# Kernel optimization log

Hardware: AMD Instinct MI355X
Metric: run time of the kernel (lower is better)

## Reference

```python
import jax, jax.numpy as jnp
import numpy as np
from jax.ops import segment_sum

N = 100000   # nodes
E = 1600000  # edges
F = 128      # node feature dim
H = 128      # hidden dim
FE = 16      # edge feature dim
G = 256      # num graphs
EPS = 1e-5   # batch-norm eps


def setup_inputs() -> dict:
    key = jax.random.key(0)
    ks = jax.random.split(key, 16)
    s = 0.05
    return {
        "x": jax.random.normal(ks[0], (N, F), jnp.float32),
        "edge_index": jax.random.randint(ks[1], (2, E), 0, N, dtype=jnp.int32),
        "edge_attr": jax.random.normal(ks[2], (E, FE), jnp.float32),
        "batch_idx": jnp.sort(jax.random.randint(ks[3], (N,), 0, G, dtype=jnp.int32)),
        # GCN layer 1
        "W_g1": jax.random.normal(ks[4], (F, H), jnp.float32) * s,
        "b_g1": jnp.zeros((H,), jnp.float32),
        "gamma1": jnp.ones((H,), jnp.float32),
        "beta1": jnp.zeros((H,), jnp.float32),
        # GCN layer 2
        "W_g2": jax.random.normal(ks[5], (H, H), jnp.float32) * s,
        "b_g2": jnp.zeros((H,), jnp.float32),
        "gamma2": jnp.ones((H,), jnp.float32),
        "beta2": jnp.zeros((H,), jnp.float32),
        # edge encoder MLP
        "W_e1": jax.random.normal(ks[6], (FE, H), jnp.float32) * s,
        "b_e1": jnp.zeros((H,), jnp.float32),
        "W_e2": jax.random.normal(ks[7], (H, H), jnp.float32) * s,
        "b_e2": jnp.zeros((H,), jnp.float32),
    }


def _gcn_bn_relu(x, src, dst, W, b, gamma, beta):
    """GCNConv (sym-normalized, self-loops) + BatchNorm1d (batch stats) + ReLU."""
    h = x @ W                                             # [N, H]
    ones = jnp.ones((E,), h.dtype)
    deg = segment_sum(ones, dst, num_segments=N) + 1.0    # self-loop degree
    dinv = jax.lax.rsqrt(deg)                             # [N]
    norm = dinv[src] * dinv[dst]                          # [E]
    agg = segment_sum(h[src] * norm[:, None], dst, num_segments=N)
    out = agg + h * (dinv * dinv)[:, None] + b            # self-loop + bias
    mu = out.mean(axis=0)
    var = out.var(axis=0)
    out = (out - mu) * jax.lax.rsqrt(var + EPS) * gamma + beta
    return jax.nn.relu(out)


def reference(x, edge_index, edge_attr, batch_idx, W_g1, b_g1, gamma1, beta1,
              W_g2, b_g2, gamma2, beta2, W_e1, b_e1, W_e2, b_e2):
    src, dst = edge_index[0], edge_index[1]
    h = _gcn_bn_relu(x, src, dst, W_g1, b_g1, gamma1, beta1)
    h = _gcn_bn_relu(h, src, dst, W_g2, b_g2, gamma2, beta2)

    # global mean pool over nodes per graph
    node_cnt = segment_sum(jnp.ones((N,), h.dtype), batch_idx, num_segments=G)
    graph_repr = segment_sum(h, batch_idx, num_segments=G) / jnp.maximum(node_cnt, 1.0)[:, None]

    # edge encoder MLP + per-graph edge mean (vectorized version of the loop)
    e = jax.nn.relu(edge_attr @ W_e1 + b_e1) @ W_e2 + b_e2   # [E, H]
    edge_batch = batch_idx[src]                              # [E]
    edge_cnt = segment_sum(jnp.ones((E,), e.dtype), edge_batch, num_segments=G)
    edge_sum = segment_sum(e, edge_batch, num_segments=G)
    edge_repr = jnp.where(edge_cnt[:, None] > 0, edge_sum / jnp.maximum(edge_cnt, 1.0)[:, None], 0.0)

    return graph_repr + edge_repr  # [G, H]
```

## Files before the change

kernel.cpp:

```cpp
#include <hip/hip_runtime.h>
#include <cstdint>

__device__ inline unsigned int bfpack2(float a, float b) {
  unsigned int ua = __float_as_uint(a), ub = __float_as_uint(b);
  ua += 0x7FFFu + ((ua >> 16) & 1u);
  ub += 0x7FFFu + ((ub >> 16) & 1u);
  return (ua >> 16) | (ub & 0xFFFF0000u);
}
__device__ inline float bflo(unsigned int u) { return __uint_as_float(u << 16); }
__device__ inline float bfhi(unsigned int u) { return __uint_as_float(u & 0xFFFF0000u); }

__global__ __launch_bounds__(256) void pre_kernel(const int* __restrict__ src,
                                                  const int* __restrict__ dst,
                                                  int* __restrict__ deg,
                                                  int* __restrict__ deg2, int nE) {
  int e = blockIdx.x * 256 + threadIdx.x;
  if (e < nE) {
    atomicAdd(&deg[dst[e]], 1);
    atomicAdd(&deg2[src[e]], 1);
  }
}

__global__ __launch_bounds__(256) void scanA_kernel(const int* __restrict__ deg,
                                                    const int* __restrict__ deg2,
                                                    int* __restrict__ rp,
                                                    int* __restrict__ rp2,
                                                    int* __restrict__ part,
                                                    int* __restrict__ part2,
                                                    int n, int nb) {
  __shared__ int sh[256];
  int b = blockIdx.x, t = threadIdx.x;
  const int* d = (b < nb) ? deg : deg2;
  int* r = (b < nb) ? rp : rp2;
  int* p = (b < nb) ? part : part2;
  int pad = (b < nb) ? 1 : 0;
  int bb = (b < nb) ? b : b - nb;
  int base = bb * 1024 + t * 4;
  int v0 = (base + 0 < n) ? d[base + 0] : 0;
  int v1 = (base + 1 < n) ? d[base + 1] : 0;
  int v2 = (base + 2 < n) ? d[base + 2] : 0;
  int v3 = (base + 3 < n) ? d[base + 3] : 0;
  if (pad) {
    v0 = (v0 + 7) & ~7; v1 = (v1 + 7) & ~7;
    v2 = (v2 + 7) & ~7; v3 = (v3 + 7) & ~7;
  }
  int ts = v0 + v1 + v2 + v3;
  sh[t] = ts;
  __syncthreads();
  for (int off = 1; off < 256; off <<= 1) {
    int x = (t >= off) ? sh[t - off] : 0;
    __syncthreads();
    sh[t] += x;
    __syncthreads();
  }
  int excl = sh[t] - ts;
  if (t == 255) p[bb] = sh[255];
  if (base + 0 < n) r[base + 0] = excl;
  if (base + 1 < n) r[base + 1] = excl + v0;
  if (base + 2 < n) r[base + 2] = excl + v0 + v1;
  if (base + 3 < n) r[base + 3] = excl + v0 + v1 + v2;
}

__global__ void scanB_kernel(int* part, int* part2, int* rp, int* rp2, int nb, int n) {
  if (threadIdx.x == 0) {
    int* p = (blockIdx.x == 0) ? part : part2;
    int* r = (blockIdx.x == 0) ? rp : rp2;
    int run = 0;
    for (int i = 0; i < nb; ++i) { int v = p[i]; p[i] = run; run += v; }
    r[n] = run;
  }
}

__global__ __launch_bounds__(256) void scanC_kernel(int* __restrict__ rp,
                                                    int* __restrict__ rp2,
                                                    const int* __restrict__ part,
                                                    const int* __restrict__ part2,
                                                    int* __restrict__ cursor,
                                                    int* __restrict__ cursor2,
                                                    const int* __restrict__ deg,
                                                    float* __restrict__ dinv, int n) {
  int i = blockIdx.x * 256 + threadIdx.x;
  if (i < n) {
    int v = rp[i] + part[i >> 10];
    rp[i] = v;
    cursor[i] = v;
    dinv[i] = rsqrtf((float)deg[i] + 1.0f);
  } else if (i < 2 * n) {
    int j = i - n;
    int v = rp2[j] + part2[j >> 10];
    rp2[j] = v;
    cursor2[j] = v;
  }
}

__global__ __launch_bounds__(256) void placepad_kernel(const int* __restrict__ src,
                                                       const int* __restrict__ dst,
                                                       const int* __restrict__ batch,
                                                       const float* __restrict__ dinv,
                                                       int* __restrict__ cursor,
                                                       int* __restrict__ cursor2,
                                                       int2* __restrict__ swv,
                                                       unsigned int* __restrict__ epk,
                                                       int* __restrict__ pos2,
                                                       const int* __restrict__ rp,
                                                       const int* __restrict__ deg,
                                                       int nE, int nN) {
  int t = blockIdx.x * 256 + threadIdx.x;
  if (t < nE) {
    int s = src[t];
    int d = dst[t];
    int p1 = atomicAdd(&cursor[d], 1);
    int2 sw; sw.x = s; sw.y = __float_as_int(dinv[s] * dinv[d]);
    swv[p1] = sw;
    int g = batch[s];
    int p2 = atomicAdd(&cursor2[s], 1);
    epk[p2] = ((unsigned int)g << 21) | (unsigned int)t;
    pos2[t] = p2;
  } else if (t < nE + nN) {
    int i = t - nE;
    int b = rp[i] + deg[i], e = rp[i + 1];
    int2 z; z.x = i; z.y = 0;
    for (int k = b; k < e; ++k) swv[k] = z;
  }
}

template <bool FUSED>
__global__ __launch_bounds__(256) void gemm128_kernel(const float* __restrict__ A,
                                                      const float* __restrict__ W,
                                                      const float* __restrict__ scale,
                                                      const float* __restrict__ shift,
                                                      unsigned int* __restrict__ hpk2,
                                                      int nrows) {
  extern __shared__ float lds[];
  float* Ws = lds;
  float* xs = lds + 128 * 128;
  const int t = threadIdx.x;
  for (int i = t; i < (128 * 128) / 4; i += 256)
    reinterpret_cast<float4*>(Ws)[i] = reinterpret_cast<const float4*>(W)[i];
  const int wave = t >> 6, lane = t & 63;
  const size_t sbase = (size_t)(lane >> 3) * (size_t)nrows * 8 + (lane & 7);
  for (int rb = blockIdx.x * 16; rb < nrows; rb += gridDim.x * 16) {
    int nr = min(16, nrows - rb);
    __syncthreads();
    for (int i = t; i < nr * 32; i += 256) {
      float4 v = reinterpret_cast<const float4*>(A + (size_t)rb * 128)[i];
      if (FUSED) {
        float4 sc4 = reinterpret_cast<const float4*>(scale)[i & 31];
        float4 sh4 = reinterpret_cast<const float4*>(shift)[i & 31];
        v.x = fmaxf(fmaf(v.x, sc4.x, sh4.x), 0.f);
        v.y = fmaxf(fmaf(v.y, sc4.y, sh4.y), 0.f);
        v.z = fmaxf(fmaf(v.z, sc4.z, sh4.z), 0.f);
        v.w = fmaxf(fmaf(v.w, sc4.w, sh4.w), 0.f);
      }
      reinterpret_cast<float4*>(xs)[i] = v;
    }
    __syncthreads();
    float acc[4][2] = {{0.f, 0.f}, {0.f, 0.f}, {0.f, 0.f}, {0.f, 0.f}};
    const float* xw = xs + wave * 4 * 128;
#pragma unroll 4
    for (int k = 0; k < 128; ++k) {
      float w0 = Ws[k * 128 + lane];
      float w1 = Ws[k * 128 + 64 + lane];
#pragma unroll
      for (int r = 0; r < 4; ++r) {
        float a = xw[r * 128 + k];
        acc[r][0] = fmaf(a, w0, acc[r][0]);
        acc[r][1] = fmaf(a, w1, acc[r][1]);
      }
    }
#pragma unroll
    for (int r = 0; r < 4; ++r) {
      int row = rb + wave * 4 + r;
      if (row < nrows)
        hpk2[sbase + (size_t)row * 8] = bfpack2(acc[r][0], acc[r][1]);
    }
  }
}

__global__ __launch_bounds__(256) void spmm8_kernel(const unsigned int* __restrict__ hpk2,
                                                    const float* __restrict__ dinv,
                                                    const int* __restrict__ rp,
                                                    const int2* __restrict__ swv,
                                                    const float* __restrict__ bias,
                                                    float* __restrict__ outp,
                                                    float* __restrict__ bnsum,
                                                    float* __restrict__ bnsq, int nN) {
  const int lane = threadIdx.x & 63;
  const int ch = lane & 7;
  const int es = lane >> 3;
  const int slice = blockIdx.x & 7;
  const unsigned int* hs = hpk2 + (size_t)slice * (size_t)nN * 8;
  const int cb = slice * 8;
  const int wib = (int)(blockIdx.x >> 3) * 4 + (int)(threadIdx.x >> 6);
  const int nws = (int)(gridDim.x >> 3) * 4;
  const unsigned long long* swq = reinterpret_cast<const unsigned long long*>(swv);
  float b0 = bias[cb + ch], b1 = bias[64 + cb + ch];
  float s0 = 0.f, s1 = 0.f, q0 = 0.f, q1 = 0.f;
  const int half = (nN + 1) >> 1;

#define SPMM_CHUNK(J, ACC0, ACC1)                                         \
  {                                                                       \
    unsigned long long v_ = __builtin_nontemporal_load(swq + (J) + es);   \
    unsigned int pp_ = hs[(size_t)(unsigned int)v_ * 8 + ch];             \
    float ww_ = __uint_as_float((unsigned int)(v_ >> 32));                \
    ACC0 = fmaf(ww_, bflo(pp_), ACC0);                                    \
    ACC1 = fmaf(ww_, bfhi(pp_), ACC1);                                    \
  }

  for (int p = wib; p < half; p += nws) {
    const int n0 = p;
    const int n1 = p + half;
    const bool has1 = n1 < nN;
    int j0 = rp[n0];
    const int end0 = rp[n0 + 1];
    int j1 = 0, end1 = 0;
    if (has1) { j1 = rp[n1]; end1 = rp[n1 + 1]; }
    float a00 = 0.f, a01 = 0.f, b00 = 0.f, b01 = 0.f;
    float a10 = 0.f, a11 = 0.f, b10 = 0.f, b11 = 0.f;
    while (j0 + 8 < end0 && j1 + 8 < end1) {
      SPMM_CHUNK(j0, a00, a01);
      SPMM_CHUNK(j0 + 8, b00, b01);
      SPMM_CHUNK(j1, a10, a11);
      SPMM_CHUNK(j1 + 8, b10, b11);
      j0 += 16; j1 += 16;
    }
    while (j0 + 8 < end0) {
      SPMM_CHUNK(j0, a00, a01);
      SPMM_CHUNK(j0 + 8, b00, b01);
      j0 += 16;
    }
    if (j0 < end0) SPMM_CHUNK(j0, a00, a01);
    while (j1 + 8 < end1) {
      SPMM_CHUNK(j1, a10, a11);
      SPMM_CHUNK(j1 + 8, b10, b11);
      j1 += 16;
    }
    if (j1 < end1) SPMM_CHUNK(j1, a10, a11);

    a00 += b00; a01 += b01;
    a10 += b10; a11 += b11;
    a00 += __shfl_xor(a00, 8);  a01 += __shfl_xor(a01, 8);
    a10 += __shfl_xor(a10, 8);  a11 += __shfl_xor(a11, 8);
    a00 += __shfl_xor(a00, 16); a01 += __shfl_xor(a01, 16);
    a10 += __shfl_xor(a10, 16); a11 += __shfl_xor(a11, 16);
    a00 += __shfl_xor(a00, 32); a01 += __shfl_xor(a01, 32);
    a10 += __shfl_xor(a10, 32); a11 += __shfl_xor(a11, 32);
    if (es == 0) {
      {
        float dn = dinv[n0];
        float sw = dn * dn;
        unsigned int pn = hs[(size_t)n0 * 8 + ch];
        float o0 = fmaf(bflo(pn), sw, a00) + b0;
        float o1 = fmaf(bfhi(pn), sw, a01) + b1;
        __builtin_nontemporal_store(o0, &outp[(size_t)n0 * 128 + cb + ch]);
        __builtin_nontemporal_store(o1, &outp[(size_t)n0 * 128 + 64 + cb + ch]);
        s0 += o0; s1 += o1;
        q0 = fmaf(o0, o0, q0); q1 = fmaf(o1, o1, q1);
      }
      if (has1) {
        float dn = dinv[n1];
        float sw = dn * dn;
        unsigned int pn = hs[(size_t)n1 * 8 + ch];
        float o0 = fmaf(bflo(pn), sw, a10) + b0;
        float o1 = fmaf(bfhi(pn), sw, a11) + b1;
        __builtin_nontemporal_store(o0, &outp[(size_t)n1 * 128 + cb + ch]);
        __builtin_nontemporal_store(o1, &outp[(size_t)n1 * 128 + 64 + cb + ch]);
        s0 += o0; s1 += o1;
        q0 = fmaf(o0, o0, q0); q1 = fmaf(o1, o1, q1);
      }
    }
  }
#undef SPMM_CHUNK
  if (es == 0) {
    atomicAdd(&bnsum[cb + ch], s0);
    atomicAdd(&bnsum[64 + cb + ch], s1);
    atomicAdd(&bnsq[cb + ch], q0);
    atomicAdd(&bnsq[64 + cb + ch], q1);
  }
}

__global__ void bnfin_kernel(const float* __restrict__ sum, const float* __restrict__ sq,
                             const float* __restrict__ gamma, const float* __restrict__ beta,
                             float* __restrict__ scale, float* __restrict__ shift,
                             float invN) {
  int c = threadIdx.x;
  float mu = sum[c] * invN;
  float var = sq[c] * invN - mu * mu;
  float sc = gamma[c] * rsqrtf(var + 1e-5f);
  scale[c] = sc;
  shift[c] = beta[c] - mu * sc;
}

__global__ __launch_bounds__(256) void pool_kernel(const float* __restrict__ h,
                                                   const int* __restrict__ batch,
                                                   const float* __restrict__ scale,
                                                   const float* __restrict__ shift,
                                                   float* __restrict__ gsum,
                                                   float* __restrict__ gcnt,
                                                   int nN, int chunk) {
  const int lane = threadIdx.x & 63;
  const int wid = (blockIdx.x * blockDim.x + threadIdx.x) >> 6;
  int beg = wid * chunk;
  if (beg >= nN) return;
  int end = min(nN, beg + chunk);
  const int c2 = 2 * lane;
  float2 sc2 = *reinterpret_cast<const float2*>(scale + c2);
  float2 sh2 = *reinterpret_cast<const float2*>(shift + c2);
  int cur = -1;
  float a0 = 0.f, a1 = 0.f, cnt = 0.f;
  for (int n = beg; n < end; ++n) {
    int g = batch[n];
    if (g != cur) {
      if (cur >= 0) {
        atomicAdd(&gsum[cur * 128 + c2], a0);
        atomicAdd(&gsum[cur * 128 + c2 + 1], a1);
        if (lane == 0) atomicAdd(&gcnt[cur], cnt);
      }
      cur = g; a0 = 0.f; a1 = 0.f; cnt = 0.f;
    }
    float2 v = *reinterpret_cast<const float2*>(h + (size_t)n * 128 + c2);
    a0 += fmaxf(fmaf(v.x, sc2.x, sh2.x), 0.f);
    a1 += fmaxf(fmaf(v.y, sc2.y, sh2.y), 0.f);
    cnt += 1.f;
  }
  if (cur >= 0) {
    atomicAdd(&gsum[cur * 128 + c2], a0);
    atomicAdd(&gsum[cur * 128 + c2 + 1], a1);
    if (lane == 0) atomicAdd(&gcnt[cur], cnt);
  }
}

__global__ __launch_bounds__(256) void scatter_kernel(const float* __restrict__ ea,
                                                      const int* __restrict__ pos2,
                                                      unsigned int* __restrict__ eah, int nE) {
  int e = blockIdx.x * 256 + threadIdx.x;
  if (e < nE) {
    const float4* p = reinterpret_cast<const float4*>(ea + (size_t)e * 16);
    float4 a = p[0], b = p[1], c = p[2], d = p[3];
    uint4 o0, o1;
    o0.x = bfpack2(a.x, a.y); o0.y = bfpack2(a.z, a.w);
    o0.z = bfpack2(b.x, b.y); o0.w = bfpack2(b.z, b.w);
    o1.x = bfpack2(c.x, c.y); o1.y = bfpack2(c.z, c.w);
    o1.z = bfpack2(d.x, d.y); o1.w = bfpack2(d.z, d.w);
    int j = pos2[e];
    uint4* dst = reinterpret_cast<uint4*>(eah + (size_t)j * 8);
    dst[0] = o0;
    dst[1] = o1;
  }
}

__global__ __launch_bounds__(256) void edge6_kernel(const unsigned int* __restrict__ eah,
                                                    const unsigned int* __restrict__ epk,
                                                    const float* __restrict__ We1,
                                                    const float* __restrict__ be1,
                                                    float* __restrict__ esum,
                                                    float* __restrict__ ecnt,
                                                    int nE, int chunk) {
  const int lane = threadIdx.x & 63;
  const int wid = (blockIdx.x * 256 + threadIdx.x) >> 6;
  int beg = wid * chunk;
  if (beg >= nE) return;
  int end = min(nE, beg + chunk);
  float w0[16], w1[16];
#pragma unroll
  for (int k = 0; k < 16; ++k) {
    w0[k] = We1[k * 128 + lane];
    w1[k] = We1[k * 128 + 64 + lane];
  }
  float b0 = be1[lane], b1 = be1[64 + lane];
  int cur = -1;
  float a0 = 0.f, a1 = 0.f, cnt = 0.f;
  const uint4* rowp = reinterpret_cast<const uint4*>(eah + (size_t)beg * 8);
  uint4 q0 = rowp[0], q1 = rowp[1];
  int g = (int)(epk[beg] >> 21);
  for (int j = beg; j < end; ++j) {
    uint4 n0, n1;
    int ng = g;
    if (j + 1 < end) {
      const uint4* np = reinterpret_cast<const uint4*>(eah + (size_t)(j + 1) * 8);
      n0 = np[0];
      n1 = np[1];
      ng = (int)(epk[j + 1] >> 21);
    }
    if (g != cur) {
      if (cur >= 0) {
        atomicAdd(&esum[cur * 128 + lane], a0);
        atomicAdd(&esum[cur * 128 + 64 + lane], a1);
        if (lane == 0) atomicAdd(&ecnt[cur], cnt);
      }
      cur = g; a0 = 0.f; a1 = 0.f; cnt = 0.f;
    }
    float u0 = b0, u1 = b1;
    float f;
    f = bflo(q0.x); u0 = fmaf(f, w0[0], u0);  u1 = fmaf(f, w1[0], u1);
    f = bfhi(q0.x); u0 = fmaf(f, w0[1], u0);  u1 = fmaf(f, w1[1], u1);
    f = bflo(q0.y); u0 = fmaf(f, w0[2], u0);  u1 = fmaf(f, w1[2], u1);
    f = bfhi(q0.y); u0 = fmaf(f, w0[3], u0);  u1 = fmaf(f, w1[3], u1);
    f = bflo(q0.z); u0 = fmaf(f, w0[4], u0);  u1 = fmaf(f, w1[4], u1);
    f = bfhi(q0.z); u0 = fmaf(f, w0[5], u0);  u1 = fmaf(f, w1[5], u1);
    f = bflo(q0.w); u0 = fmaf(f, w0[6], u0);  u1 = fmaf(f, w1[6], u1);
    f = bfhi(q0.w); u0 = fmaf(f, w0[7], u0);  u1 = fmaf(f, w1[7], u1);
    f = bflo(q1.x); u0 = fmaf(f, w0[8], u0);  u1 = fmaf(f, w1[8], u1);
    f = bfhi(q1.x); u0 = fmaf(f, w0[9], u0);  u1 = fmaf(f, w1[9], u1);
    f = bflo(q1.y); u0 = fmaf(f, w0[10], u0); u1 = fmaf(f, w1[10], u1);
    f = bfhi(q1.y); u0 = fmaf(f, w0[11], u0); u1 = fmaf(f, w1[11], u1);
    f = bflo(q1.z); u0 = fmaf(f, w0[12], u0); u1 = fmaf(f, w1[12], u1);
    f = bfhi(q1.z); u0 = fmaf(f, w0[13], u0); u1 = fmaf(f, w1[13], u1);
    f = bflo(q1.w); u0 = fmaf(f, w0[14], u0); u1 = fmaf(f, w1[14], u1);
    f = bfhi(q1.w); u0 = fmaf(f, w0[15], u0); u1 = fmaf(f, w1[15], u1);
    a0 += fmaxf(u0, 0.f);
    a1 += fmaxf(u1, 0.f);
    cnt += 1.f;
    q0 = n0; q1 = n1; g = ng;
  }
  if (cur >= 0) {
    atomicAdd(&esum[cur * 128 + lane], a0);
    atomicAdd(&esum[cur * 128 + 64 + lane], a1);
    if (lane == 0) atomicAdd(&ecnt[cur], cnt);
  }
}

__global__ __launch_bounds__(128) void final_kernel(const float* __restrict__ gsum,
                                                    const float* __restrict__ gcnt,
                                                    const float* __restrict__ esum,
                                                    const float* __restrict__ ecnt,
                                                    const float* __restrict__ We2,
                                                    const float* __restrict__ be2,
                                                    float* __restrict__ out) {
  __shared__ float row[128];
  int g = blockIdx.x, c = threadIdx.x;
  row[c] = esum[g * 128 + c];
  __syncthreads();
  float acc = 0.f;
#pragma unroll 4
  for (int k = 0; k < 128; ++k) acc = fmaf(row[k], We2[k * 128 + c], acc);
  float ce = ecnt[g];
  float er = (ce > 0.f) ? (acc / ce + be2[c]) : 0.f;
  float cn = gcnt[g];
  float gr = gsum[g * 128 + c] / fmaxf(cn, 1.f);
  out[g * 128 + c] = gr + er;
}

extern "C" void kernel_launch(void* const* d_in, const int* in_sizes, int n_in,
                              void* d_out, int out_size, void* d_ws, size_t ws_size,
                              hipStream_t stream) {
  const float* x    = (const float*)d_in[0];
  const int*   ei   = (const int*)d_in[1];
  const float* ea   = (const float*)d_in[2];
  const int*   bidx = (const int*)d_in[3];
  const float* Wg1  = (const float*)d_in[4];
  const float* bg1  = (const float*)d_in[5];
  const float* gm1  = (const float*)d_in[6];
  const float* bt1  = (const float*)d_in[7];
  const float* Wg2  = (const float*)d_in[8];
  const float* bg2  = (const float*)d_in[9];
  const float* gm2  = (const float*)d_in[10];
  const float* bt2  = (const float*)d_in[11];
  const float* We1  = (const float*)d_in[12];
  const float* be1  = (const float*)d_in[13];
  const float* We2  = (const float*)d_in[14];
  const float* be2  = (const float*)d_in[15];
  float* out = (float*)d_out;

  const int N = in_sizes[3];
  const int E = in_sizes[1] / 2;
  const int G = out_size / 128;
  const int* srcp = ei;
  const int* dstp = ei + E;
  const int Epad = E + 8 * N;

  char* w = (char*)d_ws;
  auto alloc = [&](size_t b) {
    char* p = w;
    w += (b + 15) & ~(size_t)15;
    return p;
  };
  float* bufB    = (float*)alloc((size_t)N * 128 * 4);
  unsigned int* hpk2 = (unsigned int*)alloc((size_t)N * 64 * 4);
  int2*  swv     = (int2*)alloc((size_t)Epad * 8);
  unsigned int* epk = (unsigned int*)alloc((size_t)E * 4);
  int*   pos2    = (int*)alloc((size_t)E * 4);
  int*   rp      = (int*)alloc((size_t)(N + 1) * 4);
  int*   rp2     = (int*)alloc((size_t)(N + 1) * 4);
  int*   cursor  = (int*)alloc((size_t)N * 4);
  int*   cursor2 = (int*)alloc((size_t)N * 4);
  float* dinv    = (float*)alloc((size_t)N * 4);
  char* zbase = w;
  int*   deg  = (int*)alloc((size_t)N * 4);
  int*   deg2 = (int*)alloc((size_t)N * 4);
  float* bs1  = (float*)alloc(512);
  float* bq1  = (float*)alloc(512);
  float* bs2  = (float*)alloc(512);
  float* bq2  = (float*)alloc(512);
  float* gsum = (float*)alloc((size_t)G * 128 * 4);
  float* gcnt = (float*)alloc((size_t)G * 4);
  float* esum = (float*)alloc((size_t)G * 128 * 4);
  float* ecnt = (float*)alloc((size_t)G * 4);
  int*   part  = (int*)alloc(4096);
  int*   part2 = (int*)alloc(4096);
  size_t zbytes = (size_t)(w - zbase);
  float* sc1 = (float*)alloc(512);
  float* sh1 = (float*)alloc(512);
  float* sc2 = (float*)alloc(512);
  float* sh2 = (float*)alloc(512);

  unsigned int* eah = (unsigned int*)bufB;

  hipMemsetAsync(zbase, 0, zbytes, stream);

  (void)hipFuncSetAttribute((const void*)gemm128_kernel<false>,
                            hipFuncAttributeMaxDynamicSharedMemorySize, 73728);
  (void)hipFuncSetAttribute((const void*)gemm128_kernel<true>,
                            hipFuncAttributeMaxDynamicSharedMemorySize, 73728);

  pre_kernel<<<(E + 255) / 256, 256, 0, stream>>>(srcp, dstp, deg, deg2, E);
  int nb = (N + 1023) / 1024;
  scanA_kernel<<<2 * nb, 256, 0, stream>>>(deg, deg2, rp, rp2, part, part2, N, nb);
  scanB_kernel<<<2, 64, 0, stream>>>(part, part2, rp, rp2, nb, N);
  scanC_kernel<<<(2 * N + 255) / 256, 256, 0, stream>>>(rp, rp2, part, part2, cursor,
                                                        cursor2, deg, dinv, N);
  placepad_kernel<<<(E + N + 255) / 256, 256, 0, stream>>>(srcp, dstp, bidx, dinv, cursor,
                                                           cursor2, swv, epk, pos2, rp, deg,
                                                           E, N);

  gemm128_kernel<false><<<512, 256, 73728, stream>>>(x, Wg1, nullptr, nullptr, hpk2, N);
  spmm8_kernel<<<2048, 256, 0, stream>>>(hpk2, dinv, rp, swv, bg1, bufB, bs1, bq1, N);
  bnfin_kernel<<<1, 128, 0, stream>>>(bs1, bq1, gm1, bt1, sc1, sh1, 1.0f / (float)N);

  gemm128_kernel<true><<<512, 256, 73728, stream>>>(bufB, Wg2, sc1, sh1, hpk2, N);
  spmm8_kernel<<<2048, 256, 0, stream>>>(hpk2, dinv, rp, swv, bg2, bufB, bs2, bq2, N);
  bnfin_kernel<<<1, 128, 0, stream>>>(bs2, bq2, gm2, bt2, sc2, sh2, 1.0f / (float)N);

  int nwp = (2048 * 256) / 64;
  int chunkN = (N + nwp - 1) / nwp;
  pool_kernel<<<2048, 256, 0, stream>>>(bufB, bidx, sc2, sh2, gsum, gcnt, N, chunkN);

  scatter_kernel<<<(E + 255) / 256, 256, 0, stream>>>(ea, pos2, eah, E);
  int nwe = (2048 * 256) / 64;
  int chunkE = (E + nwe - 1) / nwe;
  edge6_kernel<<<2048, 256, 0, stream>>>(eah, epk, We1, be1, esum, ecnt, E, chunkE);

  final_kernel<<<G, 128, 0, stream>>>(gsum, gcnt, esum, ecnt, We2, be2, out);
}
```

Measured before the change: 1.236 ms.

## Fold BN finalize into consumers and process four nodes per SpMM wave

Removes the two single-block bnfin kernels and computes the batch-norm scale and shift directly inside the fused GEMM (stored in LDS) and the pool kernel. This cuts two tiny launches and their serialization gaps, at the cost of redundant per-block recomputation. The SpMM loop now interleaves four destination nodes per wave with one chunk each, instead of two nodes with two chunks each. The aim is more independent gathers in flight and less tail imbalance, at the cost of more registers and extra shuffle reductions.

```diff
diff --git a/kernel.cpp b/kernel.cpp
--- a/kernel.cpp
+++ b/kernel.cpp
@@ -127,16 +127,28 @@
 template <bool FUSED>
 __global__ __launch_bounds__(256) void gemm128_kernel(const float* __restrict__ A,
                                                       const float* __restrict__ W,
-                                                      const float* __restrict__ scale,
-                                                      const float* __restrict__ shift,
+                                                      const float* __restrict__ bs,
+                                                      const float* __restrict__ bq,
+                                                      const float* __restrict__ gm,
+                                                      const float* __restrict__ bt,
+                                                      float invN,
                                                       unsigned int* __restrict__ hpk2,
                                                       int nrows) {
   extern __shared__ float lds[];
   float* Ws = lds;
   float* xs = lds + 128 * 128;
+  float* scs = xs + 16 * 128;
+  float* shs = scs + 128;
   const int t = threadIdx.x;
   for (int i = t; i < (128 * 128) / 4; i += 256)
     reinterpret_cast<float4*>(Ws)[i] = reinterpret_cast<const float4*>(W)[i];
+  if (FUSED && t < 128) {
+    float mu = bs[t] * invN;
+    float var = bq[t] * invN - mu * mu;
+    float sc = gm[t] * rsqrtf(var + 1e-5f);
+    scs[t] = sc;
+    shs[t] = bt[t] - mu * sc;
+  }
   const int wave = t >> 6, lane = t & 63;
   const size_t sbase = (size_t)(lane >> 3) * (size_t)nrows * 8 + (lane & 7);
   for (int rb = blockIdx.x * 16; rb < nrows; rb += gridDim.x * 16) {
@@ -145,8 +157,8 @@
     for (int i = t; i < nr * 32; i += 256) {
       float4 v = reinterpret_cast<const float4*>(A + (size_t)rb * 128)[i];
       if (FUSED) {
-        float4 sc4 = reinterpret_cast<const float4*>(scale)[i & 31];
-        float4 sh4 = reinterpret_cast<const float4*>(shift)[i & 31];
+        float4 sc4 = reinterpret_cast<const float4*>(scs)[i & 31];
+        float4 sh4 = reinterpret_cast<const float4*>(shs)[i & 31];
         v.x = fmaxf(fmaf(v.x, sc4.x, sh4.x), 0.f);
         v.y = fmaxf(fmaf(v.y, sc4.y, sh4.y), 0.f);
         v.z = fmaxf(fmaf(v.z, sc4.z, sh4.z), 0.f);
@@ -196,7 +208,7 @@
   const unsigned long long* swq = reinterpret_cast<const unsigned long long*>(swv);
   float b0 = bias[cb + ch], b1 = bias[64 + cb + ch];
   float s0 = 0.f, s1 = 0.f, q0 = 0.f, q1 = 0.f;
-  const int half = (nN + 1) >> 1;
+  const int qn = (nN + 3) >> 2;
 
 #define SPMM_CHUNK(J, ACC0, ACC1)                                         \
   {                                                                       \
@@ -206,71 +218,72 @@
     ACC0 = fmaf(ww_, bflo(pp_), ACC0);                                    \
     ACC1 = fmaf(ww_, bfhi(pp_), ACC1);                                    \
   }
-
-  for (int p = wib; p < half; p += nws) {
-    const int n0 = p;
-    const int n1 = p + half;
-    const bool has1 = n1 < nN;
-    int j0 = rp[n0];
-    const int end0 = rp[n0 + 1];
-    int j1 = 0, end1 = 0;
-    if (has1) { j1 = rp[n1]; end1 = rp[n1 + 1]; }
-    float a00 = 0.f, a01 = 0.f, b00 = 0.f, b01 = 0.f;
-    float a10 = 0.f, a11 = 0.f, b10 = 0.f, b11 = 0.f;
-    while (j0 + 8 < end0 && j1 + 8 < end1) {
+#define SPMM_EPI(NI, A0, A1)                                              \
+  {                                                                       \
+    float dn_ = dinv[NI];                                                 \
+    float sw_ = dn_ * dn_;                                                \
+    unsigned int pn_ = hs[(size_t)(NI) * 8 + ch];                         \
+    float o0_ = fmaf(bflo(pn_), sw_, A0) + b0;                            \
+    float o1_ = fmaf(bfhi(pn_), sw_, A1) + b1;                            \
+    __builtin_nontemporal_store(o0_, &outp[(size_t)(NI) * 128 + cb + ch]);\
+    __builtin_nontemporal_store(o1_, &outp[(size_t)(NI) * 128 + 64 + cb + ch]); \
+    s0 += o0_; s1 += o1_;                                                 \
+    q0 = fmaf(o0_, o0_, q0); q1 = fmaf(o1_, o1_, q1);                     \
+  }
+
+  for (int p = wib; p < qn; p += nws) {
+    const int n0 = p, n1 = p + qn, n2 = p + 2 * qn, n3 = p + 3 * qn;
+    const bool v1 = n1 < nN, v2 = n2 < nN, v3 = n3 < nN;
+    int j0 = rp[n0], e0 = rp[n0 + 1];
+    int j1 = 0, e1 = 0, j2 = 0, e2 = 0, j3 = 0, e3 = 0;
+    if (v1) { j1 = rp[n1]; e1 = rp[n1 + 1]; }
+    if (v2) { j2 = rp[n2]; e2 = rp[n2 + 1]; }
+    if (v3) { j3 = rp[n3]; e3 = rp[n3 + 1]; }
+    float a00 = 0.f, a01 = 0.f, a10 = 0.f, a11 = 0.f;
+    float a20 = 0.f, a21 = 0.f, a30 = 0.f, a31 = 0.f;
+    while (j0 < e0 && j1 < e1 && j2 < e2 && j3 < e3) {
       SPMM_CHUNK(j0, a00, a01);
-      SPMM_CHUNK(j0 + 8, b00, b01);
       SPMM_CHUNK(j1, a10, a11);
-      SPMM_CHUNK(j1 + 8, b10, b11);
-      j0 += 16; j1 += 16;
-    }
-    while (j0 + 8 < end0) {
+      SPMM_CHUNK(j2, a20, a21);
+      SPMM_CHUNK(j3, a30, a31);
+      j0 += 8; j1 += 8; j2 += 8; j3 += 8;
+    }
+    while (j0 < e0 && j1 < e1) {
       SPMM_CHUNK(j0, a00, a01);
-      SPMM_CHUNK(j0 + 8, b00, b01);
-      j0 += 16;
-    }
-    if (j0 < end0) SPMM_CHUNK(j0, a00, a01);
-    while (j1 + 8 < end1) {
       SPMM_CHUNK(j1, a10, a11);
-      SPMM_CHUNK(j1 + 8, b10, b11);
-      j1 += 16;
-    }
-    if (j1 < end1) SPMM_CHUNK(j1, a10, a11);
-
-    a00 += b00; a01 += b01;
-    a10 += b10; a11 += b11;
+      j0 += 8; j1 += 8;
+    }
+    while (j2 < e2 && j3 < e3) {
+      SPMM_CHUNK(j2, a20, a21);
+      SPMM_CHUNK(j3, a30, a31);
+      j2 += 8; j3 += 8;
+    }
+    while (j0 < e0) { SPMM_CHUNK(j0, a00, a01); j0 += 8; }
+    while (j1 < e1) { SPMM_CHUNK(j1, a10, a11); j1 += 8; }
+    while (j2 < e2) { SPMM_CHUNK(j2, a20, a21); j2 += 8; }
+    while (j3 < e3) { SPMM_CHUNK(j3, a30, a31); j3 += 8; }
+
     a00 += __shfl_xor(a00, 8);  a01 += __shfl_xor(a01, 8);
     a10 += __shfl_xor(a10, 8);  a11 += __shfl_xor(a11, 8);
+    a20 += __shfl_xor(a20, 8);  a21 += __shfl_xor(a21, 8);
+    a30 += __shfl_xor(a30, 8);  a31 += __shfl_xor(a31, 8);
     a00 += __shfl_xor(a00, 16); a01 += __shfl_xor(a01, 16);
     a10 += __shfl_xor(a10, 16); a11 += __shfl_xor(a11, 16);
+    a20 += __shfl_xor(a20, 16); a21 += __shfl_xor(a21, 16);
+    a30 += __shfl_xor(a30, 16); a31 += __shfl_xor(a31, 16);
     a00 += __shfl_xor(a00, 32); a01 += __shfl_xor(a01, 32);
     a10 += __shfl_xor(a10, 32); a11 += __shfl_xor(a11, 32);
+    a20 += __shfl_xor(a20, 32); a21 += __shfl_xor(a21, 32);
+    a30 += __shfl_xor(a30, 32); a31 += __shfl_xor(a31, 32);
     if (es == 0) {
-      {
-        float dn = dinv[n0];
-        float sw = dn * dn;
-        unsigned int pn = hs[(size_t)n0 * 8 + ch];
-        float o0 = fmaf(bflo(pn), sw, a00) + b0;
-        float o1 = fmaf(bfhi(pn), sw, a01) + b1;
-        __builtin_nontemporal_store(o0, &outp[(size_t)n0 * 128 + cb + ch]);
-        __builtin_nontemporal_store(o1, &outp[(size_t)n0 * 128 + 64 + cb + ch]);
-        s0 += o0; s1 += o1;
-        q0 = fmaf(o0, o0, q0); q1 = fmaf(o1, o1, q1);
-      }
-      if (has1) {
-        float dn = dinv[n1];
-        float sw = dn * dn;
-        unsigned int pn = hs[(size_t)n1 * 8 + ch];
-        float o0 = fmaf(bflo(pn), sw, a10) + b0;
-        float o1 = fmaf(bfhi(pn), sw, a11) + b1;
-        __builtin_nontemporal_store(o0, &outp[(size_t)n1 * 128 + cb + ch]);
-        __builtin_nontemporal_store(o1, &outp[(size_t)n1 * 128 + 64 + cb + ch]);
-        s0 += o0; s1 += o1;
-        q0 = fmaf(o0, o0, q0); q1 = fmaf(o1, o1, q1);
-      }
+      SPMM_EPI(n0, a00, a01);
+      if (v1) SPMM_EPI(n1, a10, a11);
+      if (v2) SPMM_EPI(n2, a20, a21);
+      if (v3) SPMM_EPI(n3, a30, a31);
     }
   }
 #undef SPMM_CHUNK
+#undef SPMM_EPI
   if (es == 0) {
     atomicAdd(&bnsum[cb + ch], s0);
     atomicAdd(&bnsum[64 + cb + ch], s1);
@@ -279,22 +292,13 @@
   }
 }
 
-__global__ void bnfin_kernel(const float* __restrict__ sum, const float* __restrict__ sq,
-                             const float* __restrict__ gamma, const float* __restrict__ beta,
-                             float* __restrict__ scale, float* __restrict__ shift,
-                             float invN) {
-  int c = threadIdx.x;
-  float mu = sum[c] * invN;
-  float var = sq[c] * invN - mu * mu;
-  float sc = gamma[c] * rsqrtf(var + 1e-5f);
-  scale[c] = sc;
-  shift[c] = beta[c] - mu * sc;
-}
-
 __global__ __launch_bounds__(256) void pool_kernel(const float* __restrict__ h,
                                                    const int* __restrict__ batch,
-                                                   const float* __restrict__ scale,
-                                                   const float* __restrict__ shift,
+                                                   const float* __restrict__ bs,
+                                                   const float* __restrict__ bq,
+                                                   const float* __restrict__ gm,
+                                                   const float* __restrict__ bt,
+                                                   float invN,
                                                    float* __restrict__ gsum,
                                                    float* __restrict__ gcnt,
                                                    int nN, int chunk) {
@@ -304,8 +308,10 @@
   if (beg >= nN) return;
   int end = min(nN, beg + chunk);
   const int c2 = 2 * lane;
-  float2 sc2 = *reinterpret_cast<const float2*>(scale + c2);
-  float2 sh2 = *reinterpret_cast<const float2*>(shift + c2);
+  float mu0 = bs[c2] * invN, mu1 = bs[c2 + 1] * invN;
+  float va0 = bq[c2] * invN - mu0 * mu0, va1 = bq[c2 + 1] * invN - mu1 * mu1;
+  float sc0 = gm[c2] * rsqrtf(va0 + 1e-5f), sc1v = gm[c2 + 1] * rsqrtf(va1 + 1e-5f);
+  float sh0 = bt[c2] - mu0 * sc0, sh1v = bt[c2 + 1] - mu1 * sc1v;
   int cur = -1;
   float a0 = 0.f, a1 = 0.f, cnt = 0.f;
   for (int n = beg; n < end; ++n) {
@@ -319,8 +325,8 @@
       cur = g; a0 = 0.f; a1 = 0.f; cnt = 0.f;
     }
     float2 v = *reinterpret_cast<const float2*>(h + (size_t)n * 128 + c2);
-    a0 += fmaxf(fmaf(v.x, sc2.x, sh2.x), 0.f);
-    a1 += fmaxf(fmaf(v.y, sc2.y, sh2.y), 0.f);
+    a0 += fmaxf(fmaf(v.x, sc0, sh0), 0.f);
+    a1 += fmaxf(fmaf(v.y, sc1v, sh1v), 0.f);
     cnt += 1.f;
   }
   if (cur >= 0) {
@@ -499,19 +505,15 @@
   int*   part  = (int*)alloc(4096);
   int*   part2 = (int*)alloc(4096);
   size_t zbytes = (size_t)(w - zbase);
-  float* sc1 = (float*)alloc(512);
-  float* sh1 = (float*)alloc(512);
-  float* sc2 = (float*)alloc(512);
-  float* sh2 = (float*)alloc(512);
 
   unsigned int* eah = (unsigned int*)bufB;
 
   hipMemsetAsync(zbase, 0, zbytes, stream);
 
   (void)hipFuncSetAttribute((const void*)gemm128_kernel<false>,
-                            hipFuncAttributeMaxDynamicSharedMemorySize, 73728);
+                            hipFuncAttributeMaxDynamicSharedMemorySize, 74752);
   (void)hipFuncSetAttribute((const void*)gemm128_kernel<true>,
-                            hipFuncAttributeMaxDynamicSharedMemorySize, 73728);
+                            hipFuncAttributeMaxDynamicSharedMemorySize, 74752);
 
   pre_kernel<<<(E + 255) / 256, 256, 0, stream>>>(srcp, dstp, deg, deg2, E);
   int nb = (N + 1023) / 1024;
@@ -523,17 +525,20 @@
                                                            cursor2, swv, epk, pos2, rp, deg,
                                                            E, N);
 
-  gemm128_kernel<false><<<512, 256, 73728, stream>>>(x, Wg1, nullptr, nullptr, hpk2, N);
+  const float invN = 1.0f / (float)N;
+
+  gemm128_kernel<false><<<512, 256, 74752, stream>>>(x, Wg1, nullptr, nullptr, nullptr,
+                                                     nullptr, 0.f, hpk2, N);
   spmm8_kernel<<<2048, 256, 0, stream>>>(hpk2, dinv, rp, swv, bg1, bufB, bs1, bq1, N);
-  bnfin_kernel<<<1, 128, 0, stream>>>(bs1, bq1, gm1, bt1, sc1, sh1, 1.0f / (float)N);
-
-  gemm128_kernel<true><<<512, 256, 73728, stream>>>(bufB, Wg2, sc1, sh1, hpk2, N);
+
+  gemm128_kernel<true><<<512, 256, 74752, stream>>>(bufB, Wg2, bs1, bq1, gm1, bt1, invN,
+                                                    hpk2, N);
   spmm8_kernel<<<2048, 256, 0, stream>>>(hpk2, dinv, rp, swv, bg2, bufB, bs2, bq2, N);
-  bnfin_kernel<<<1, 128, 0, stream>>>(bs2, bq2, gm2, bt2, sc2, sh2, 1.0f / (float)N);
 
   int nwp = (2048 * 256) / 64;
   int chunkN = (N + nwp - 1) / nwp;
-  pool_kernel<<<2048, 256, 0, stream>>>(bufB, bidx, sc2, sh2, gsum, gcnt, N, chunkN);
+  pool_kernel<<<2048, 256, 0, stream>>>(bufB, bidx, bs2, bq2, gm2, bt2, invN,
+                                        gsum, gcnt, N, chunkN);
 
   scatter_kernel<<<(E + 255) / 256, 256, 0, stream>>>(ea, pos2, eah, E);
   int nwe = (2048 * 256) / 64;
```

New measurement: 1.472 ms. 19.1% more time.
